# Optimization experiments

Measured on AMD Instinct MI355X. Metric: run time of the kernel, lower is better.

Reference implementation:

```python
import jax, jax.numpy as jnp
import numpy as np

N, E, IN, H, OUT, G = 100000, 1600000, 9, 64, 6, 1024
EPS = 1e-5


def setup_inputs() -> dict:
    key = jax.random.key(0)
    ks = jax.random.split(key, 24)
    inp = {
        "x": jax.random.normal(ks[0], (N, IN), dtype=jnp.float32),
        "edge_index": jax.random.randint(ks[1], (2, E), 0, N, dtype=jnp.int64),
        "edge_weight": jax.random.uniform(ks[2], (E,), dtype=jnp.float32),
        "batch": jnp.sort(jax.random.randint(ks[3], (N,), 0, G, dtype=jnp.int64)),
    }
    def lin(k, fan_in, fan_out):
        return jax.random.normal(k, (fan_in, fan_out), dtype=jnp.float32) / np.sqrt(fan_in)
    # GraphConv layer 0: IN -> H; layers 1,2: H -> H
    inp["W_rel0"], inp["W_root0"], inp["b0"] = lin(ks[4], IN, H), lin(ks[5], IN, H), jnp.zeros((H,), jnp.float32)
    inp["W_rel1"], inp["W_root1"], inp["b1"] = lin(ks[6], H, H), lin(ks[7], H, H), jnp.zeros((H,), jnp.float32)
    inp["W_rel2"], inp["W_root2"], inp["b2"] = lin(ks[8], H, H), lin(ks[9], H, H), jnp.zeros((H,), jnp.float32)
    # BatchNorm params for the first num_layers-1 = 2 layers
    inp["g0"], inp["be0"] = jnp.ones((H,), jnp.float32), jnp.zeros((H,), jnp.float32)
    inp["g1"], inp["be1"] = jnp.ones((H,), jnp.float32), jnp.zeros((H,), jnp.float32)
    # MLP head
    inp["W_l1"], inp["b_l1"] = lin(ks[10], H, H), jnp.zeros((H,), jnp.float32)
    inp["W_l2"], inp["b_l2"] = lin(ks[11], H, OUT), jnp.zeros((OUT,), jnp.float32)
    return inp


def graph_conv(x, src, dst, ew, W_rel, W_root, b):
    # PyG GraphConv: out = aggr_add(e_ji * x_j) @ W_rel + b + x @ W_root
    msg = x[src] * ew[:, None]                      # [E, F] gather
    agg = jax.ops.segment_sum(msg, dst, num_segments=x.shape[0])  # [N, F] scatter-add
    return agg @ W_rel + b + x @ W_root


def batch_norm(x, g, b):
    m = jnp.mean(x, axis=0)
    v = jnp.var(x, axis=0)
    return (x - m) * jax.lax.rsqrt(v + EPS) * g + b


def reference(x, edge_index, edge_weight, batch,
              W_rel0, W_root0, b0, W_rel1, W_root1, b1, W_rel2, W_root2, b2,
              g0, be0, g1, be1, W_l1, b_l1, W_l2, b_l2):
    src, dst = edge_index[0], edge_index[1]
    # layer 0: conv -> BN -> relu (dropout p applied only in training; eval here)
    h = graph_conv(x, src, dst, edge_weight, W_rel0, W_root0, b0)
    h = jax.nn.relu(batch_norm(h, g0, be0))
    # layer 1
    h = graph_conv(h, src, dst, edge_weight, W_rel1, W_root1, b1)
    h = jax.nn.relu(batch_norm(h, g1, be1))
    # layer 2 (no norm/relu)
    h = graph_conv(h, src, dst, edge_weight, W_rel2, W_root2, b2)
    # global mean pool over graphs
    summed = jax.ops.segment_sum(h, batch, num_segments=G)            # [G, H]
    counts = jax.ops.segment_sum(jnp.ones((h.shape[0],), h.dtype), batch, num_segments=G)
    pooled = summed / jnp.maximum(counts, 1.0)[:, None]
    # MLP head
    z = jax.nn.relu(pooled @ W_l1 + b_l1)
    return z @ W_l2 + b_l2
```

## Files before the change

### kernel.cpp

```cpp
#include <hip/hip_runtime.h>
#include <hip/hip_fp16.h>

constexpr int N    = 100000;
constexpr int E    = 1600000;
constexpr int FIN  = 9;
constexpr int OUTF = 6;
constexpr int G    = 1024;
constexpr int NPB  = 256;
constexpr int NB   = (N + NPB - 1) / NPB;
constexpr int CH   = 2048;
constexpr int NCH  = (E + CH - 1) / CH;
constexpr int BCAP = 4864;
constexpr int CBCAP= BCAP + NPB + 8;
constexpr int EBUF = 5888;
constexpr int ZCNT = 256 + G * 64;

typedef _Float16 f16x8 __attribute__((ext_vector_type(8)));
typedef float    f32x4 __attribute__((ext_vector_type(4)));

__device__ __forceinline__ void atomAddF(float* p, float v) { unsafeAtomicAdd(p, v); }

__device__ __forceinline__ float us2f(unsigned short u) {
    return __half2float(__builtin_bit_cast(__half, u));
}

__global__ __launch_bounds__(256) void initK(int* __restrict__ cursor, float* __restrict__ zeros,
    const float* __restrict__ x, __half* __restrict__ x9)
{
    int i = blockIdx.x * 256 + threadIdx.x;
    if (i < NB) cursor[i] = i * BCAP;
    if (i < ZCNT) zeros[i] = 0.f;
    if (i < N * FIN) x9[i] = __float2half(x[i]);
}

__global__ __launch_bounds__(256) void passA(const int* __restrict__ src, const int* __restrict__ dst,
    const float* __restrict__ ew, int* __restrict__ cursor, int2* __restrict__ bucketed)
{
    __shared__ int h[NB];
    __shared__ int hb[NB];
    int t = threadIdx.x;
    for (int i = t; i < NB; i += 256) h[i] = 0;
    __syncthreads();
    int base = blockIdx.x * CH;
    int myS[8], myD[8], rk[8]; float myW[8];
#pragma unroll
    for (int i = 0; i < 8; i++) {
        int e = base + i * 256 + t;
        if (e < E) {
            myS[i] = src[e]; myD[i] = dst[e]; myW[i] = ew[e];
            rk[i] = atomicAdd(&h[myD[i] >> 8], 1);
        } else myD[i] = -1;
    }
    __syncthreads();
    for (int i = t; i < NB; i += 256) hb[i] = h[i] ? atomicAdd(&cursor[i], h[i]) : 0;
    __syncthreads();
#pragma unroll
    for (int i = 0; i < 8; i++) if (myD[i] >= 0) {
        int packed = myS[i] | ((myD[i] & 255) << 24);
        bucketed[hb[myD[i] >> 8] + rk[i]] = make_int2(packed, __float_as_int(myW[i]));
    }
}

__global__ __launch_bounds__(NPB) void passB(const int* __restrict__ cursor,
    const int2* __restrict__ bucketed, int* __restrict__ ebeg, int* __restrict__ eend,
    int2* __restrict__ csr)
{
    __shared__ int2 ebuf[EBUF];
    __shared__ int cl[NPB], sa[NPB], sb[NPB], curs[NPB];
    int b = blockIdx.x, t = threadIdx.x;
    int node0 = b * NPB;
    int nnode = min(NPB, N - node0);
    int cnt = cursor[b] - b * BCAP;
    int abase = b * BCAP;
    int base = b * CBCAP;
    bool fits = (cnt <= EBUF);
    cl[t] = 0;
    __syncthreads();
    for (int e = t; e < cnt; e += NPB) {
        int2 r = bucketed[abase + e];
        if (fits) ebuf[e] = r;
        atomicAdd(&cl[((unsigned)r.x) >> 24], 1);
    }
    __syncthreads();
    int deg = cl[t];
    int pc = (deg + 1) & ~1;
    int* cur = sa; int* nxt = sb;
    cur[t] = pc;
    __syncthreads();
    for (int o = 1; o < NPB; o <<= 1) {
        int v = cur[t];
        if (t >= o) v += cur[t - o];
        nxt[t] = v;
        __syncthreads();
        int* tmp = cur; cur = nxt; nxt = tmp;
    }
    int off = cur[t] - pc;
    if (t < nnode) { ebeg[node0 + t] = base + off; eend[node0 + t] = base + off + deg; }
    curs[t] = off;
    __syncthreads();
    for (int e = t; e < cnt; e += NPB) {
        int2 r = fits ? ebuf[e] : bucketed[abase + e];
        int dl = ((unsigned)r.x) >> 24;
        int pos = base + atomicAdd(&curs[dl], 1);
        csr[pos] = make_int2(r.x & 0x00FFFFFF, r.y);
    }
    __syncthreads();
    if (t < nnode && (deg & 1)) csr[base + off + deg] = make_int2(0, 0);
    if (t < 4) csr[base + cur[NPB - 1] + t] = make_int2(0, 0);
}

__global__ __launch_bounds__(256) void wprep(const float* __restrict__ Wrel1, const float* __restrict__ Wroot1,
    const float* __restrict__ Wrel2, const float* __restrict__ Wroot2, __half* __restrict__ Wt)
{
    int i = blockIdx.x * 256 + threadIdx.x;
    int layer = i >> 13, r = i & 8191;
    int c = r >> 6, k = r & 63;
    const float* Wrel = layer ? Wrel2 : Wrel1;
    const float* Wroot = layer ? Wroot2 : Wroot1;
    float v = (c < 64) ? Wrel[k * 64 + c] : Wroot[k * 64 + (c - 64)];
    Wt[i] = __float2half(v);
}

__global__ __launch_bounds__(256, 2) void gather9(const __half* __restrict__ x9h,
    const int2* __restrict__ csr, const int* __restrict__ ebeg, const int* __restrict__ eend,
    float* __restrict__ agg9)
{
    const unsigned short* __restrict__ x9 = (const unsigned short*)x9h;
    int t = threadIdx.x, lane = t & 63;
    int es = lane >> 4, fc = min(lane & 15, FIN - 1);
    int wv = __builtin_amdgcn_readfirstlane((blockIdx.x * blockDim.x + t) >> 6);
    int nw = (gridDim.x * blockDim.x) >> 6;
    for (int n = wv; n < N; n += nw) {
        int beg = ebeg[n], end = eend[n];
        int last = end - 1;
        int2 eA0 = csr[min(beg + es,      last)];
        int2 eB0 = csr[min(beg + 4 + es,  last)];
        int2 eA1 = csr[min(beg + 8 + es,  last)];
        int2 eB1 = csr[min(beg + 12 + es, last)];
        unsigned short xA = x9[(size_t)eA0.x * FIN + fc];
        unsigned short xB = x9[(size_t)eB0.x * FIN + fc];
        float a0 = 0.f, a1 = 0.f;
        for (int k = beg; k < end; k += 8) {
            int2 eA2 = csr[min(k + 16 + es, last)];
            int2 eB2 = csr[min(k + 20 + es, last)];
            unsigned short nxA = x9[(size_t)eA1.x * FIN + fc];
            unsigned short nxB = x9[(size_t)eB1.x * FIN + fc];
            float wA = (k + es     < end) ? __int_as_float(eA0.y) : 0.f;
            float wB = (k + 4 + es < end) ? __int_as_float(eB0.y) : 0.f;
            a0 = fmaf(wA, us2f(xA), a0);
            a1 = fmaf(wB, us2f(xB), a1);
            eA0 = eA1; eB0 = eB1; eA1 = eA2; eB1 = eB2;
            xA = nxA; xB = nxB;
        }
        float r = a0 + a1;
        r += __shfl(r, lane ^ 16, 64);
        r += __shfl(r, lane ^ 32, 64);
        if (lane < FIN) agg9[(size_t)n * FIN + lane] = r;
    }
}

__global__ __launch_bounds__(256) void proj0post(const float* __restrict__ x,
    const float* __restrict__ agg9, const float* __restrict__ Wrel,
    const float* __restrict__ Wroot, const float* __restrict__ bias,
    __half* __restrict__ H0, float* __restrict__ stats)
{
    int t = threadIdx.x, j = t & 63;
    int nl = __builtin_amdgcn_readfirstlane(t >> 6);
    float wrel[FIN], wroot[FIN];
#pragma unroll
    for (int k = 0; k < FIN; k++) { wrel[k] = Wrel[k * 64 + j]; wroot[k] = Wroot[k * 64 + j]; }
    float bj = bias[j];
    float s1 = 0.f, s2 = 0.f;
    const int ntiles = N / 4;
    for (int tile = blockIdx.x; tile < ntiles; tile += gridDim.x) {
        int n = tile * 4 + nl;
        const float* xr = x + (size_t)n * FIN;
        const float* ar = agg9 + (size_t)n * FIN;
        float acc = bj;
#pragma unroll
        for (int k = 0; k < FIN; k++) {
            acc = fmaf(ar[k], wrel[k], acc);
            acc = fmaf(xr[k], wroot[k], acc);
        }
        H0[(size_t)n * 64 + j] = __float2half(acc);
        s1 += acc; s2 += acc * acc;
    }
    __shared__ float sred[256];
    sred[t] = s1; __syncthreads();
    if (t < 64) atomAddF(&stats[t], sred[t] + sred[t+64] + sred[t+128] + sred[t+192]);
    __syncthreads();
    sred[t] = s2; __syncthreads();
    if (t < 64) atomAddF(&stats[64 + t], sred[t] + sred[t+64] + sred[t+128] + sred[t+192]);
}

__global__ __launch_bounds__(256) void projm(const __half* __restrict__ Hin, const __half* __restrict__ Wt,
    const float* __restrict__ bias, const float* __restrict__ stats,
    const float* __restrict__ gam, const float* __restrict__ bet,
    __half* __restrict__ P, __half* __restrict__ Hout)
{
    int t = threadIdx.x, lane = t & 63;
    int wv = blockIdx.x * 4 + (t >> 6);
    int nw = gridDim.x * 4;
    int n16 = lane & 15, quad = lane >> 4;
    constexpr float invN = 1.0f / (float)N;
    float sc[16], sh[16];
#pragma unroll
    for (int jj = 0; jj < 16; jj++) {
        int k = (jj < 8) ? (quad * 8 + jj) : (32 + quad * 8 + (jj - 8));
        float m = stats[k] * invN;
        float v = stats[64 + k] * invN - m * m;
        sc[jj] = gam[k] * rsqrtf(v + 1e-5f);
        sh[jj] = bet[k] - m * sc[jj];
    }
    f16x8 bf[8][2];
#pragma unroll
    for (int ct = 0; ct < 8; ct++)
#pragma unroll
        for (int kh = 0; kh < 2; kh++)
            bf[ct][kh] = *(const f16x8*)(Wt + (size_t)(ct * 16 + n16) * 64 + kh * 32 + quad * 8);
    float bcol[4];
#pragma unroll
    for (int i = 0; i < 4; i++) bcol[i] = bias[i * 16 + n16];
    const int NT = N / 16;
    for (int tile = wv; tile < NT; tile += nw) {
        int n0 = tile * 16;
        f16x8 r0 = *(const f16x8*)(Hin + (size_t)(n0 + n16) * 64 + quad * 8);
        f16x8 r1 = *(const f16x8*)(Hin + (size_t)(n0 + n16) * 64 + 32 + quad * 8);
        f16x8 a0, a1;
#pragma unroll
        for (int jj = 0; jj < 8; jj++) {
            a0[jj] = (_Float16)fmaxf(fmaf((float)r0[jj], sc[jj],     sh[jj]),     0.f);
            a1[jj] = (_Float16)fmaxf(fmaf((float)r1[jj], sc[jj + 8], sh[jj + 8]), 0.f);
        }
        f32x4 acc[8];
#pragma unroll
        for (int ct = 0; ct < 8; ct++) {
            f32x4 c = {0.f, 0.f, 0.f, 0.f};
            c = __builtin_amdgcn_mfma_f32_16x16x32_f16(a0, bf[ct][0], c, 0, 0, 0);
            c = __builtin_amdgcn_mfma_f32_16x16x32_f16(a1, bf[ct][1], c, 0, 0, 0);
            acc[ct] = c;
        }
#pragma unroll
        for (int ct = 0; ct < 8; ct++) {
#pragma unroll
            for (int r = 0; r < 4; r++) {
                int n = n0 + quad * 4 + r;
                if (ct < 4) P[(size_t)n * 64 + ct * 16 + n16] = __float2half(acc[ct][r]);
                else Hout[(size_t)n * 64 + (ct - 4) * 16 + n16] = __float2half(acc[ct][r] + bcol[ct - 4]);
            }
        }
    }
}

template<int EPI>
__global__ __launch_bounds__(256, 2) void gather(const __half* __restrict__ Ph, __half* H,
    const int2* __restrict__ csr, const int* __restrict__ ebeg, const int* __restrict__ eend,
    float* __restrict__ stats, const int* __restrict__ batch, float* __restrict__ pool)
{
    const unsigned short* __restrict__ P = (const unsigned short*)Ph;
    int t = threadIdx.x, lane = t & 63;
    int wv = __builtin_amdgcn_readfirstlane((blockIdx.x * blockDim.x + t) >> 6);
    int nw = (gridDim.x * blockDim.x) >> 6;
    float s1 = 0.f, s2 = 0.f;
    const int NPAIR = N / 2;
    for (int pr = wv; pr < NPAIR; pr += nw) {
        int n0 = 2 * pr, n1 = n0 + 1;
        int b0 = ebeg[n0], m0 = (eend[n0] - b0 + 1) >> 1;
        int b1 = ebeg[n1], m1 = (eend[n1] - b1 + 1) >> 1;
        const int4* q0 = (const int4*)csr + (b0 >> 1);
        const int4* q1 = (const int4*)csr + (b1 >> 1);
        int c0 = max(m0 - 1, 0), c1 = max(m1 - 1, 0);
        float x0 = __half2float(H[(size_t)n0 * 64 + lane]);
        float x1 = __half2float(H[(size_t)n1 * 64 + lane]);
        int4 qaA = q0[0],          qbA = q0[min(1, c0)];
        int4 qcA = q1[0],          qdA = q1[min(1, c1)];
        int4 qaB = q0[min(2, c0)], qbB = q0[min(3, c0)];
        int4 qcB = q1[min(2, c1)], qdB = q1[min(3, c1)];
        int4 qaC = q0[min(4, c0)], qbC = q0[min(5, c0)];
        int4 qcC = q1[min(4, c1)], qdC = q1[min(5, c1)];
        unsigned short pa0 = P[(size_t)qaA.x * 64 + lane], pa1 = P[(size_t)qaA.z * 64 + lane];
        unsigned short pb0 = P[(size_t)qbA.x * 64 + lane], pb1 = P[(size_t)qbA.z * 64 + lane];
        unsigned short pc0 = P[(size_t)qcA.x * 64 + lane], pc1 = P[(size_t)qcA.z * 64 + lane];
        unsigned short pd0 = P[(size_t)qdA.x * 64 + lane], pd1 = P[(size_t)qdA.z * 64 + lane];
        unsigned short na0 = P[(size_t)qaB.x * 64 + lane], na1 = P[(size_t)qaB.z * 64 + lane];
        unsigned short nb0 = P[(size_t)qbB.x * 64 + lane], nb1 = P[(size_t)qbB.z * 64 + lane];
        unsigned short nc0 = P[(size_t)qcB.x * 64 + lane], nc1 = P[(size_t)qcB.z * 64 + lane];
        unsigned short nd0 = P[(size_t)qdB.x * 64 + lane], nd1 = P[(size_t)qdB.z * 64 + lane];
        float a0 = 0.f, a1 = 0.f, a2 = 0.f, a3 = 0.f;
        float a4 = 0.f, a5 = 0.f, a6 = 0.f, a7 = 0.f;
        int mm = max(m0, m1);
        for (int k = 0; k < mm; k += 2) {
            int4 qaD = q0[min(k + 6, c0)], qbD = q0[min(k + 7, c0)];
            int4 qcD = q1[min(k + 6, c1)], qdD = q1[min(k + 7, c1)];
            unsigned short ma0 = P[(size_t)qaC.x * 64 + lane], ma1 = P[(size_t)qaC.z * 64 + lane];
            unsigned short mb0 = P[(size_t)qbC.x * 64 + lane], mb1 = P[(size_t)qbC.z * 64 + lane];
            unsigned short mc0 = P[(size_t)qcC.x * 64 + lane], mc1 = P[(size_t)qcC.z * 64 + lane];
            unsigned short md0 = P[(size_t)qdC.x * 64 + lane], md1 = P[(size_t)qdC.z * 64 + lane];
            float wa = (k     < m0) ? __int_as_float(qaA.y) : 0.f;
            float wA = (k     < m0) ? __int_as_float(qaA.w) : 0.f;
            float wb = (k + 1 < m0) ? __int_as_float(qbA.y) : 0.f;
            float wB = (k + 1 < m0) ? __int_as_float(qbA.w) : 0.f;
            float wc = (k     < m1) ? __int_as_float(qcA.y) : 0.f;
            float wC = (k     < m1) ? __int_as_float(qcA.w) : 0.f;
            float wd = (k + 1 < m1) ? __int_as_float(qdA.y) : 0.f;
            float wD = (k + 1 < m1) ? __int_as_float(qdA.w) : 0.f;
            a0 = fmaf(wa, us2f(pa0), a0); a1 = fmaf(wA, us2f(pa1), a1);
            a2 = fmaf(wb, us2f(pb0), a2); a3 = fmaf(wB, us2f(pb1), a3);
            a4 = fmaf(wc, us2f(pc0), a4); a5 = fmaf(wC, us2f(pc1), a5);
            a6 = fmaf(wd, us2f(pd0), a6); a7 = fmaf(wD, us2f(pd1), a7);
            qaA = qaB; qbA = qbB; qcA = qcB; qdA = qdB;
            qaB = qaC; qbB = qbC; qcB = qcC; qdB = qdC;
            qaC = qaD; qbC = qbD; qcC = qcD; qdC = qdD;
            pa0 = na0; pa1 = na1; pb0 = nb0; pb1 = nb1;
            pc0 = nc0; pc1 = nc1; pd0 = nd0; pd1 = nd1;
            na0 = ma0; na1 = ma1; nb0 = mb0; nb1 = mb1;
            nc0 = mc0; nc1 = mc1; nd0 = md0; nd1 = md1;
        }
        float r0 = x0 + ((a0 + a2) + (a1 + a3));
        float r1 = x1 + ((a4 + a6) + (a5 + a7));
        if constexpr (EPI == 0) {
            H[(size_t)n0 * 64 + lane] = __float2half(r0);
            H[(size_t)n1 * 64 + lane] = __float2half(r1);
            s1 += r0 + r1; s2 += r0 * r0 + r1 * r1;
        } else {
            atomAddF(&pool[batch[n0] * 64 + lane], r0);
            atomAddF(&pool[batch[n1] * 64 + lane], r1);
        }
    }
    if constexpr (EPI == 0) {
        __shared__ float sred[256];
        sred[t] = s1; __syncthreads();
        if (t < 64) atomAddF(&stats[t], sred[t] + sred[t+64] + sred[t+128] + sred[t+192]);
        __syncthreads();
        sred[t] = s2; __syncthreads();
        if (t < 64) atomAddF(&stats[64 + t], sred[t] + sred[t+64] + sred[t+128] + sred[t+192]);
    }
}

__global__ __launch_bounds__(64) void head(const float* __restrict__ pool,
    const int* __restrict__ batch, const float* __restrict__ Wl1, const float* __restrict__ bl1,
    const float* __restrict__ Wl2, const float* __restrict__ bl2, float* __restrict__ out)
{
    int g = blockIdx.x, t = threadIdx.x;
    __shared__ float sp[64];
    __shared__ float sz[64];
    __shared__ int scnt;
    if (t == 0) {
        int lo = 0, hi = N;
        while (lo < hi) { int m = (lo + hi) >> 1; if (batch[m] < g) lo = m + 1; else hi = m; }
        int lo2 = lo, hi2 = N;
        while (lo2 < hi2) { int m = (lo2 + hi2) >> 1; if (batch[m] < g + 1) lo2 = m + 1; else hi2 = m; }
        scnt = lo2 - lo;
    }
    __syncthreads();
    float cnt = fmaxf((float)scnt, 1.0f);
    sp[t] = pool[g * 64 + t] / cnt;
    __syncthreads();
    float acc = bl1[t];
#pragma unroll
    for (int k = 0; k < 64; k++) acc = fmaf(sp[k], Wl1[k * 64 + t], acc);
    sz[t] = fmaxf(acc, 0.f);
    __syncthreads();
    if (t < OUTF) {
        float o = bl2[t];
#pragma unroll
        for (int k = 0; k < 64; k++) o = fmaf(sz[k], Wl2[k * OUTF + t], o);
        out[g * OUTF + t] = o;
    }
}

extern "C" void kernel_launch(void* const* d_in, const int* in_sizes, int n_in,
                              void* d_out, int out_size, void* d_ws, size_t ws_size,
                              hipStream_t stream)
{
    const float* x     = (const float*)d_in[0];
    const int*   ei    = (const int*)d_in[1];
    const float* ew    = (const float*)d_in[2];
    const int*   batch = (const int*)d_in[3];
    const float* Wrel0 = (const float*)d_in[4];
    const float* Wroot0= (const float*)d_in[5];
    const float* b0    = (const float*)d_in[6];
    const float* Wrel1 = (const float*)d_in[7];
    const float* Wroot1= (const float*)d_in[8];
    const float* b1    = (const float*)d_in[9];
    const float* Wrel2 = (const float*)d_in[10];
    const float* Wroot2= (const float*)d_in[11];
    const float* b2    = (const float*)d_in[12];
    const float* g0    = (const float*)d_in[13];
    const float* be0   = (const float*)d_in[14];
    const float* g1    = (const float*)d_in[15];
    const float* be1   = (const float*)d_in[16];
    const float* Wl1   = (const float*)d_in[17];
    const float* bl1   = (const float*)d_in[18];
    const float* Wl2   = (const float*)d_in[19];
    const float* bl2   = (const float*)d_in[20];
    const int* srcI = ei;
    const int* dstI = ei + E;

    __half* Ha     = (__half*)d_ws;
    __half* Hb     = Ha + (size_t)N * 64;
    __half* P      = Hb + (size_t)N * 64;
    int2*   csr    = (int2*)(P + (size_t)N * 64);
    int*    ebeg   = (int*)(csr + (size_t)NB * CBCAP);
    int*    eend   = ebeg + N;
    int*    cursor = eend + N;
    float*  stats0 = (float*)(cursor + NB);
    float*  stats1 = stats0 + 128;
    float*  pool   = stats1 + 128;
    __half* Wt1    = (__half*)(pool + G * 64);
    __half* Wt2    = Wt1 + 128 * 64;
    float*  agg9   = (float*)(Wt2 + 128 * 64);
    __half* x9     = (__half*)(agg9 + (size_t)N * FIN);
    int2*   bucketed = (int2*)Ha;

    initK<<<(N * FIN + 255) / 256, 256, 0, stream>>>(cursor, stats0, x, x9);
    passA<<<NCH, 256, 0, stream>>>(srcI, dstI, ew, cursor, bucketed);
    passB<<<NB, NPB, 0, stream>>>(cursor, bucketed, ebeg, eend, csr);
    wprep<<<64, 256, 0, stream>>>(Wrel1, Wroot1, Wrel2, Wroot2, Wt1);

    gather9<<<2048, 256, 0, stream>>>(x9, csr, ebeg, eend, agg9);
    proj0post<<<2048, 256, 0, stream>>>(x, agg9, Wrel0, Wroot0, b0, Ha, stats0);

    projm<<<1024, 256, 0, stream>>>(Ha, Wt1, b1, stats0, g0, be0, P, Hb);
    gather<0><<<2048, 256, 0, stream>>>(P, Hb, csr, ebeg, eend, stats1, nullptr, nullptr);

    projm<<<1024, 256, 0, stream>>>(Hb, Wt2, b2, stats1, g1, be1, P, Ha);
    gather<1><<<2048, 256, 0, stream>>>(P, Ha, csr, ebeg, eend, nullptr, batch, pool);

    head<<<G, 64, 0, stream>>>(pool, batch, Wl1, bl1, Wl2, bl2, (float*)d_out);
}
```

Baseline: 468.7 us.

## Stream gathered neighbor rows into LDS ring via global_load_lds pipeline

Rewrites the gather kernel so each wavefront runs a software-pipelined producer/consumer ring in shared memory. It issues direct global-to-LDS loads of neighbor feature rows (4 edges per step, GLK steps ahead) and consumes them after an explicit vmcnt wait. The old code held register-resident prefetch of two nodes at a time. The new scheme handles one node per iteration with a continuous cross-node prefetch stream, aiming to keep more memory requests in flight while cutting register pressure. The fixed vmcnt(8) count depends on exactly which loads are outstanding, so it is fragile. The extra LDS traffic and the dropped occupancy hint may also cost throughput.

```diff
diff --git a/kernel.cpp b/kernel.cpp
--- a/kernel.cpp
+++ b/kernel.cpp
@@ -22,6 +22,11 @@
 
 __device__ __forceinline__ float us2f(unsigned short u) {
     return __half2float(__builtin_bit_cast(__half, u));
+}
+
+__device__ __forceinline__ void gll4(const void* g, void* l) {
+    __builtin_amdgcn_global_load_lds((const __attribute__((address_space(1))) void*)g,
+                                     (__attribute__((address_space(3))) void*)l, 4, 0, 0);
 }
 
 __global__ __launch_bounds__(256) void initK(int* __restrict__ cursor, float* __restrict__ zeros,
@@ -252,83 +257,99 @@
     }
 }
 
+constexpr int GLK = 4;
+constexpr int GRS = 8;
+
 template<int EPI>
-__global__ __launch_bounds__(256, 2) void gather(const __half* __restrict__ Ph, __half* H,
+__global__ __launch_bounds__(256) void gather(const __half* __restrict__ Ph, __half* H,
     const int2* __restrict__ csr, const int* __restrict__ ebeg, const int* __restrict__ eend,
     float* __restrict__ stats, const int* __restrict__ batch, float* __restrict__ pool)
 {
-    const unsigned short* __restrict__ P = (const unsigned short*)Ph;
-    int t = threadIdx.x, lane = t & 63;
+    __shared__ unsigned short ring[4][GRS][256];
+    __shared__ int4 pring[4][GRS][2];
+    __shared__ float sred[256];
+    int t = threadIdx.x, lane = t & 63, w = t >> 6;
+    unsigned short* myring = &ring[w][0][0];
+    int4* mypring = &pring[w][0][0];
+    const char* Pb = (const char*)Ph;
+    const int4* csr4 = (const int4*)csr;
     int wv = __builtin_amdgcn_readfirstlane((blockIdx.x * blockDim.x + t) >> 6);
     int nw = (gridDim.x * blockDim.x) >> 6;
+    int l31 = (lane & 31) * 4;
+
+    int pn = pn = wv, ppb = 0, ppm = 0, pnq = 0, pq = 0;
+    {
+        int b = ebeg[pn]; ppb = b >> 1; ppm = (eend[pn] - b + 1) >> 1; pnq = (ppm + 1) >> 1;
+        while (pnq == 0) {
+            pn += nw; if (pn >= N) break;
+            int b2 = ebeg[pn]; ppb = b2 >> 1; ppm = (eend[pn] - b2 + 1) >> 1; pnq = (ppm + 1) >> 1;
+        }
+    }
+    auto produceStep = [&](int slot) {
+        if (pn < N) {
+            int lastpk = ppb + ppm - 1;
+            int4 pk0 = csr4[min(ppb + 2 * pq,     lastpk)];
+            int4 pk1 = csr4[min(ppb + 2 * pq + 1, lastpk)];
+            int r0 = (lane < 32) ? pk0.x : pk0.z;
+            int r1 = (lane < 32) ? pk1.x : pk1.z;
+            gll4(Pb + (size_t)r0 * 128 + l31, myring + slot * 256);
+            gll4(Pb + (size_t)r1 * 128 + l31, myring + slot * 256 + 128);
+            if (lane < 2) mypring[slot * 2 + lane] = lane ? pk1 : pk0;
+            pq++;
+            if (pq >= pnq) {
+                pq = 0;
+                do {
+                    pn += nw; if (pn >= N) break;
+                    int b = ebeg[pn]; ppb = b >> 1; ppm = (eend[pn] - b + 1) >> 1; pnq = (ppm + 1) >> 1;
+                } while (pnq == 0);
+            }
+        } else {
+            gll4(Pb + l31, myring + slot * 256);
+            gll4(Pb + l31, myring + slot * 256 + 128);
+        }
+    };
+
+    int qp = 0, qc = 0;
+    for (int i = 0; i < GLK; i++) { produceStep(qp & (GRS - 1)); qp++; }
+
     float s1 = 0.f, s2 = 0.f;
-    const int NPAIR = N / 2;
-    for (int pr = wv; pr < NPAIR; pr += nw) {
-        int n0 = 2 * pr, n1 = n0 + 1;
-        int b0 = ebeg[n0], m0 = (eend[n0] - b0 + 1) >> 1;
-        int b1 = ebeg[n1], m1 = (eend[n1] - b1 + 1) >> 1;
-        const int4* q0 = (const int4*)csr + (b0 >> 1);
-        const int4* q1 = (const int4*)csr + (b1 >> 1);
-        int c0 = max(m0 - 1, 0), c1 = max(m1 - 1, 0);
-        float x0 = __half2float(H[(size_t)n0 * 64 + lane]);
-        float x1 = __half2float(H[(size_t)n1 * 64 + lane]);
-        int4 qaA = q0[0],          qbA = q0[min(1, c0)];
-        int4 qcA = q1[0],          qdA = q1[min(1, c1)];
-        int4 qaB = q0[min(2, c0)], qbB = q0[min(3, c0)];
-        int4 qcB = q1[min(2, c1)], qdB = q1[min(3, c1)];
-        int4 qaC = q0[min(4, c0)], qbC = q0[min(5, c0)];
-        int4 qcC = q1[min(4, c1)], qdC = q1[min(5, c1)];
-        unsigned short pa0 = P[(size_t)qaA.x * 64 + lane], pa1 = P[(size_t)qaA.z * 64 + lane];
-        unsigned short pb0 = P[(size_t)qbA.x * 64 + lane], pb1 = P[(size_t)qbA.z * 64 + lane];
-        unsigned short pc0 = P[(size_t)qcA.x * 64 + lane], pc1 = P[(size_t)qcA.z * 64 + lane];
-        unsigned short pd0 = P[(size_t)qdA.x * 64 + lane], pd1 = P[(size_t)qdA.z * 64 + lane];
-        unsigned short na0 = P[(size_t)qaB.x * 64 + lane], na1 = P[(size_t)qaB.z * 64 + lane];
-        unsigned short nb0 = P[(size_t)qbB.x * 64 + lane], nb1 = P[(size_t)qbB.z * 64 + lane];
-        unsigned short nc0 = P[(size_t)qcB.x * 64 + lane], nc1 = P[(size_t)qcB.z * 64 + lane];
-        unsigned short nd0 = P[(size_t)qdB.x * 64 + lane], nd1 = P[(size_t)qdB.z * 64 + lane];
-        float a0 = 0.f, a1 = 0.f, a2 = 0.f, a3 = 0.f;
-        float a4 = 0.f, a5 = 0.f, a6 = 0.f, a7 = 0.f;
-        int mm = max(m0, m1);
-        for (int k = 0; k < mm; k += 2) {
-            int4 qaD = q0[min(k + 6, c0)], qbD = q0[min(k + 7, c0)];
-            int4 qcD = q1[min(k + 6, c1)], qdD = q1[min(k + 7, c1)];
-            unsigned short ma0 = P[(size_t)qaC.x * 64 + lane], ma1 = P[(size_t)qaC.z * 64 + lane];
-            unsigned short mb0 = P[(size_t)qbC.x * 64 + lane], mb1 = P[(size_t)qbC.z * 64 + lane];
-            unsigned short mc0 = P[(size_t)qcC.x * 64 + lane], mc1 = P[(size_t)qcC.z * 64 + lane];
-            unsigned short md0 = P[(size_t)qdC.x * 64 + lane], md1 = P[(size_t)qdC.z * 64 + lane];
-            float wa = (k     < m0) ? __int_as_float(qaA.y) : 0.f;
-            float wA = (k     < m0) ? __int_as_float(qaA.w) : 0.f;
-            float wb = (k + 1 < m0) ? __int_as_float(qbA.y) : 0.f;
-            float wB = (k + 1 < m0) ? __int_as_float(qbA.w) : 0.f;
-            float wc = (k     < m1) ? __int_as_float(qcA.y) : 0.f;
-            float wC = (k     < m1) ? __int_as_float(qcA.w) : 0.f;
-            float wd = (k + 1 < m1) ? __int_as_float(qdA.y) : 0.f;
-            float wD = (k + 1 < m1) ? __int_as_float(qdA.w) : 0.f;
-            a0 = fmaf(wa, us2f(pa0), a0); a1 = fmaf(wA, us2f(pa1), a1);
-            a2 = fmaf(wb, us2f(pb0), a2); a3 = fmaf(wB, us2f(pb1), a3);
-            a4 = fmaf(wc, us2f(pc0), a4); a5 = fmaf(wC, us2f(pc1), a5);
-            a6 = fmaf(wd, us2f(pd0), a6); a7 = fmaf(wD, us2f(pd1), a7);
-            qaA = qaB; qbA = qbB; qcA = qcB; qdA = qdB;
-            qaB = qaC; qbB = qbC; qcB = qcC; qdB = qdC;
-            qaC = qaD; qbC = qbD; qcC = qcD; qdC = qdD;
-            pa0 = na0; pa1 = na1; pb0 = nb0; pb1 = nb1;
-            pc0 = nc0; pc1 = nc1; pd0 = nd0; pd1 = nd1;
-            na0 = ma0; na1 = ma1; nb0 = mb0; nb1 = mb1;
-            nc0 = mc0; nc1 = mc1; nd0 = md0; nd1 = md1;
-        }
-        float r0 = x0 + ((a0 + a2) + (a1 + a3));
-        float r1 = x1 + ((a4 + a6) + (a5 + a7));
+    for (int cn = wv; cn < N; cn += nw) {
+        int b = ebeg[cn];
+        int cm = (eend[cn] - b + 1) >> 1;
+        int cnq = (cm + 1) >> 1;
+        float xr = __half2float(H[(size_t)cn * 64 + lane]);
+        float acc = 0.f;
+        for (int q = 0; q < cnq; q++) {
+            produceStep(qp & (GRS - 1)); qp++;
+            int slot = qc & (GRS - 1); qc++;
+            asm volatile("s_waitcnt vmcnt(8)" ::: "memory");
+            int4 pk0 = mypring[slot * 2];
+            int4 pk1 = mypring[slot * 2 + 1];
+            const unsigned short* s = myring + slot * 256;
+            float v0 = us2f(s[lane]);
+            float v1 = us2f(s[64 + lane]);
+            float v2 = us2f(s[128 + lane]);
+            float v3 = us2f(s[192 + lane]);
+            float w0 = (2 * q     < cm) ? __int_as_float(pk0.y) : 0.f;
+            float w1 = (2 * q     < cm) ? __int_as_float(pk0.w) : 0.f;
+            float w2 = (2 * q + 1 < cm) ? __int_as_float(pk1.y) : 0.f;
+            float w3 = (2 * q + 1 < cm) ? __int_as_float(pk1.w) : 0.f;
+            acc = fmaf(w0, v0, acc);
+            acc = fmaf(w1, v1, acc);
+            acc = fmaf(w2, v2, acc);
+            acc = fmaf(w3, v3, acc);
+        }
+        float r = xr + acc;
         if constexpr (EPI == 0) {
-            H[(size_t)n0 * 64 + lane] = __float2half(r0);
-            H[(size_t)n1 * 64 + lane] = __float2half(r1);
-            s1 += r0 + r1; s2 += r0 * r0 + r1 * r1;
+            H[(size_t)cn * 64 + lane] = __float2half(r);
+            s1 += r; s2 += r * r;
         } else {
-            atomAddF(&pool[batch[n0] * 64 + lane], r0);
-            atomAddF(&pool[batch[n1] * 64 + lane], r1);
-        }
-    }
+            atomAddF(&pool[batch[cn] * 64 + lane], r);
+        }
+    }
+    asm volatile("s_waitcnt vmcnt(0)" ::: "memory");
+
     if constexpr (EPI == 0) {
-        __shared__ float sred[256];
         sred[t] = s1; __syncthreads();
         if (t < 64) atomAddF(&stats[t], sred[t] + sred[t+64] + sred[t+128] + sred[t+192]);
         __syncthreads();
```

Result: slower. 687.3 us (+46.6%).

## Partition each node's edges into source slices and gather slice-by-slice for locality

Applied to the files above, without the earlier changes.

The CSR build now sorts each node's edges into four source-index slices, each padded to even length, and records the slice boundaries per node. The 64-wide gather kernels make each wave own 13 nodes and walk them slice by slice, so all waves touch the same quarter of P at the same time. This should improve L2/MALL hit rates for the random row gathers. It also pads x9 to 16 halves per row so gather9 uses aligned row addresses, at the cost of extra padding edges, a more complex passB, and lower memory-level parallelism per wave in the gather loop.

```diff
diff --git a/kernel.cpp b/kernel.cpp
--- a/kernel.cpp
+++ b/kernel.cpp
@@ -11,7 +11,9 @@
 constexpr int CH   = 2048;
 constexpr int NCH  = (E + CH - 1) / CH;
 constexpr int BCAP = 4864;
-constexpr int CBCAP= BCAP + NPB + 8;
+constexpr int NSLC = 4;
+constexpr int SLCW = (N + NSLC - 1) / NSLC;
+constexpr int CBCAP= BCAP + NPB * NSLC + 8;
 constexpr int EBUF = 5888;
 constexpr int ZCNT = 256 + G * 64;
 
@@ -30,7 +32,10 @@
     int i = blockIdx.x * 256 + threadIdx.x;
     if (i < NB) cursor[i] = i * BCAP;
     if (i < ZCNT) zeros[i] = 0.f;
-    if (i < N * FIN) x9[i] = __float2half(x[i]);
+    if (i < N * 16) {
+        int n = i >> 4, f = i & 15;
+        x9[i] = __float2half(f < FIN ? x[n * FIN + f] : 0.f);
+    }
 }
 
 __global__ __launch_bounds__(256) void passA(const int* __restrict__ src, const int* __restrict__ dst,
@@ -63,10 +68,11 @@
 
 __global__ __launch_bounds__(NPB) void passB(const int* __restrict__ cursor,
     const int2* __restrict__ bucketed, int* __restrict__ ebeg, int* __restrict__ eend,
-    int2* __restrict__ csr)
+    int4* __restrict__ segpk, int2* __restrict__ csr)
 {
     __shared__ int2 ebuf[EBUF];
-    __shared__ int cl[NPB], sa[NPB], sb[NPB], curs[NPB];
+    __shared__ int cl4[NPB][NSLC];
+    __shared__ int sa[NPB], sb[NPB];
     int b = blockIdx.x, t = threadIdx.x;
     int node0 = b * NPB;
     int nnode = min(NPB, N - node0);
@@ -74,16 +80,19 @@
     int abase = b * BCAP;
     int base = b * CBCAP;
     bool fits = (cnt <= EBUF);
-    cl[t] = 0;
+#pragma unroll
+    for (int s = 0; s < NSLC; s++) cl4[t][s] = 0;
     __syncthreads();
     for (int e = t; e < cnt; e += NPB) {
         int2 r = bucketed[abase + e];
         if (fits) ebuf[e] = r;
-        atomicAdd(&cl[((unsigned)r.x) >> 24], 1);
-    }
-    __syncthreads();
-    int deg = cl[t];
-    int pc = (deg + 1) & ~1;
+        int src = r.x & 0x00FFFFFF;
+        atomicAdd(&cl4[((unsigned)r.x) >> 24][src / SLCW], 1);
+    }
+    __syncthreads();
+    int d0 = cl4[t][0], d1 = cl4[t][1], d2 = cl4[t][2], d3 = cl4[t][3];
+    int p0 = (d0 + 1) & ~1, p1 = (d1 + 1) & ~1, p2 = (d2 + 1) & ~1, p3 = (d3 + 1) & ~1;
+    int pc = p0 + p1 + p2 + p3;
     int* cur = sa; int* nxt = sb;
     cur[t] = pc;
     __syncthreads();
@@ -95,17 +104,31 @@
         int* tmp = cur; cur = nxt; nxt = tmp;
     }
     int off = cur[t] - pc;
-    if (t < nnode) { ebeg[node0 + t] = base + off; eend[node0 + t] = base + off + deg; }
-    curs[t] = off;
+    if (t < nnode) {
+        ebeg[node0 + t] = base + off;
+        eend[node0 + t] = base + off + pc;
+        segpk[node0 + t] = make_int4(p0 >> 1, (p0 + p1) >> 1,
+                                     (p0 + p1 + p2) >> 1, pc >> 1);
+    }
+    cl4[t][0] = off;
+    cl4[t][1] = off + p0;
+    cl4[t][2] = off + p0 + p1;
+    cl4[t][3] = off + p0 + p1 + p2;
     __syncthreads();
     for (int e = t; e < cnt; e += NPB) {
         int2 r = fits ? ebuf[e] : bucketed[abase + e];
         int dl = ((unsigned)r.x) >> 24;
-        int pos = base + atomicAdd(&curs[dl], 1);
-        csr[pos] = make_int2(r.x & 0x00FFFFFF, r.y);
-    }
-    __syncthreads();
-    if (t < nnode && (deg & 1)) csr[base + off + deg] = make_int2(0, 0);
+        int src = r.x & 0x00FFFFFF;
+        int pos = base + atomicAdd(&cl4[dl][src / SLCW], 1);
+        csr[pos] = make_int2(src, r.y);
+    }
+    __syncthreads();
+    if (t < nnode) {
+        if (d0 & 1) csr[base + cl4[t][0]] = make_int2(0, 0);
+        if (d1 & 1) csr[base + cl4[t][1]] = make_int2(0, 0);
+        if (d2 & 1) csr[base + cl4[t][2]] = make_int2(0, 0);
+        if (d3 & 1) csr[base + cl4[t][3]] = make_int2(0, 0);
+    }
     if (t < 4) csr[base + cur[NPB - 1] + t] = make_int2(0, 0);
 }
 
@@ -127,7 +150,7 @@
 {
     const unsigned short* __restrict__ x9 = (const unsigned short*)x9h;
     int t = threadIdx.x, lane = t & 63;
-    int es = lane >> 4, fc = min(lane & 15, FIN - 1);
+    int es = lane >> 4, fc = lane & 15;
     int wv = __builtin_amdgcn_readfirstlane((blockIdx.x * blockDim.x + t) >> 6);
     int nw = (gridDim.x * blockDim.x) >> 6;
     for (int n = wv; n < N; n += nw) {
@@ -137,14 +160,14 @@
         int2 eB0 = csr[min(beg + 4 + es,  last)];
         int2 eA1 = csr[min(beg + 8 + es,  last)];
         int2 eB1 = csr[min(beg + 12 + es, last)];
-        unsigned short xA = x9[(size_t)eA0.x * FIN + fc];
-        unsigned short xB = x9[(size_t)eB0.x * FIN + fc];
+        unsigned short xA = x9[(size_t)eA0.x * 16 + fc];
+        unsigned short xB = x9[(size_t)eB0.x * 16 + fc];
         float a0 = 0.f, a1 = 0.f;
         for (int k = beg; k < end; k += 8) {
             int2 eA2 = csr[min(k + 16 + es, last)];
             int2 eB2 = csr[min(k + 20 + es, last)];
-            unsigned short nxA = x9[(size_t)eA1.x * FIN + fc];
-            unsigned short nxB = x9[(size_t)eB1.x * FIN + fc];
+            unsigned short nxA = x9[(size_t)eA1.x * 16 + fc];
+            unsigned short nxB = x9[(size_t)eB1.x * 16 + fc];
             float wA = (k + es     < end) ? __int_as_float(eA0.y) : 0.f;
             float wB = (k + 4 + es < end) ? __int_as_float(eB0.y) : 0.f;
             a0 = fmaf(wA, us2f(xA), a0);
@@ -254,85 +277,60 @@
 
 template<int EPI>
 __global__ __launch_bounds__(256, 2) void gather(const __half* __restrict__ Ph, __half* H,
-    const int2* __restrict__ csr, const int* __restrict__ ebeg, const int* __restrict__ eend,
+    const int2* __restrict__ csr, const int* __restrict__ ebeg, const int4* __restrict__ segpk,
     float* __restrict__ stats, const int* __restrict__ batch, float* __restrict__ pool)
 {
     const unsigned short* __restrict__ P = (const unsigned short*)Ph;
     int t = threadIdx.x, lane = t & 63;
     int wv = __builtin_amdgcn_readfirstlane((blockIdx.x * blockDim.x + t) >> 6);
     int nw = (gridDim.x * blockDim.x) >> 6;
-    float s1 = 0.f, s2 = 0.f;
-    const int NPAIR = N / 2;
-    for (int pr = wv; pr < NPAIR; pr += nw) {
-        int n0 = 2 * pr, n1 = n0 + 1;
-        int b0 = ebeg[n0], m0 = (eend[n0] - b0 + 1) >> 1;
-        int b1 = ebeg[n1], m1 = (eend[n1] - b1 + 1) >> 1;
-        const int4* q0 = (const int4*)csr + (b0 >> 1);
-        const int4* q1 = (const int4*)csr + (b1 >> 1);
-        int c0 = max(m0 - 1, 0), c1 = max(m1 - 1, 0);
-        float x0 = __half2float(H[(size_t)n0 * 64 + lane]);
-        float x1 = __half2float(H[(size_t)n1 * 64 + lane]);
-        int4 qaA = q0[0],          qbA = q0[min(1, c0)];
-        int4 qcA = q1[0],          qdA = q1[min(1, c1)];
-        int4 qaB = q0[min(2, c0)], qbB = q0[min(3, c0)];
-        int4 qcB = q1[min(2, c1)], qdB = q1[min(3, c1)];
-        int4 qaC = q0[min(4, c0)], qbC = q0[min(5, c0)];
-        int4 qcC = q1[min(4, c1)], qdC = q1[min(5, c1)];
-        unsigned short pa0 = P[(size_t)qaA.x * 64 + lane], pa1 = P[(size_t)qaA.z * 64 + lane];
-        unsigned short pb0 = P[(size_t)qbA.x * 64 + lane], pb1 = P[(size_t)qbA.z * 64 + lane];
-        unsigned short pc0 = P[(size_t)qcA.x * 64 + lane], pc1 = P[(size_t)qcA.z * 64 + lane];
-        unsigned short pd0 = P[(size_t)qdA.x * 64 + lane], pd1 = P[(size_t)qdA.z * 64 + lane];
-        unsigned short na0 = P[(size_t)qaB.x * 64 + lane], na1 = P[(size_t)qaB.z * 64 + lane];
-        unsigned short nb0 = P[(size_t)qbB.x * 64 + lane], nb1 = P[(size_t)qbB.z * 64 + lane];
-        unsigned short nc0 = P[(size_t)qcB.x * 64 + lane], nc1 = P[(size_t)qcB.z * 64 + lane];
-        unsigned short nd0 = P[(size_t)qdB.x * 64 + lane], nd1 = P[(size_t)qdB.z * 64 + lane];
-        float a0 = 0.f, a1 = 0.f, a2 = 0.f, a3 = 0.f;
-        float a4 = 0.f, a5 = 0.f, a6 = 0.f, a7 = 0.f;
-        int mm = max(m0, m1);
-        for (int k = 0; k < mm; k += 2) {
-            int4 qaD = q0[min(k + 6, c0)], qbD = q0[min(k + 7, c0)];
-            int4 qcD = q1[min(k + 6, c1)], qdD = q1[min(k + 7, c1)];
-            unsigned short ma0 = P[(size_t)qaC.x * 64 + lane], ma1 = P[(size_t)qaC.z * 64 + lane];
-            unsigned short mb0 = P[(size_t)qbC.x * 64 + lane], mb1 = P[(size_t)qbC.z * 64 + lane];
-            unsigned short mc0 = P[(size_t)qcC.x * 64 + lane], mc1 = P[(size_t)qcC.z * 64 + lane];
-            unsigned short md0 = P[(size_t)qdC.x * 64 + lane], md1 = P[(size_t)qdC.z * 64 + lane];
-            float wa = (k     < m0) ? __int_as_float(qaA.y) : 0.f;
-            float wA = (k     < m0) ? __int_as_float(qaA.w) : 0.f;
-            float wb = (k + 1 < m0) ? __int_as_float(qbA.y) : 0.f;
-            float wB = (k + 1 < m0) ? __int_as_float(qbA.w) : 0.f;
-            float wc = (k     < m1) ? __int_as_float(qcA.y) : 0.f;
-            float wC = (k     < m1) ? __int_as_float(qcA.w) : 0.f;
-            float wd = (k + 1 < m1) ? __int_as_float(qdA.y) : 0.f;
-            float wD = (k + 1 < m1) ? __int_as_float(qdA.w) : 0.f;
-            a0 = fmaf(wa, us2f(pa0), a0); a1 = fmaf(wA, us2f(pa1), a1);
-            a2 = fmaf(wb, us2f(pb0), a2); a3 = fmaf(wB, us2f(pb1), a3);
-            a4 = fmaf(wc, us2f(pc0), a4); a5 = fmaf(wC, us2f(pc1), a5);
-            a6 = fmaf(wd, us2f(pd0), a6); a7 = fmaf(wD, us2f(pd1), a7);
-            qaA = qaB; qbA = qbB; qcA = qcB; qdA = qdB;
-            qaB = qaC; qbB = qbC; qcB = qcC; qdB = qdC;
-            qaC = qaD; qbC = qbD; qcC = qcD; qdC = qdD;
-            pa0 = na0; pa1 = na1; pb0 = nb0; pb1 = nb1;
-            pc0 = nc0; pc1 = nc1; pd0 = nd0; pd1 = nd1;
-            na0 = ma0; na1 = ma1; nb0 = mb0; nb1 = mb1;
-            nc0 = mc0; nc1 = mc1; nd0 = md0; nd1 = md1;
-        }
-        float r0 = x0 + ((a0 + a2) + (a1 + a3));
-        float r1 = x1 + ((a4 + a6) + (a5 + a7));
-        if constexpr (EPI == 0) {
-            H[(size_t)n0 * 64 + lane] = __float2half(r0);
-            H[(size_t)n1 * 64 + lane] = __float2half(r1);
-            s1 += r0 + r1; s2 += r0 * r0 + r1 * r1;
-        } else {
-            atomAddF(&pool[batch[n0] * 64 + lane], r0);
-            atomAddF(&pool[batch[n1] * 64 + lane], r1);
+    constexpr int NN = 13;
+    float acc[NN];
+#pragma unroll
+    for (int i = 0; i < NN; i++) acc[i] = 0.f;
+    const int4* csr4 = (const int4*)csr;
+#pragma unroll
+    for (int p = 0; p < NSLC; p++) {
+#pragma unroll
+        for (int i = 0; i < NN; i++) {
+            int n = wv + i * nw;
+            if (n < N) {
+                int e4 = ebeg[n] >> 1;
+                int4 pf = segpk[n];
+                int s0 = (p == 0) ? 0 : (p == 1 ? pf.x : p == 2 ? pf.y : pf.z);
+                int s1 = (p == 0) ? pf.x : (p == 1 ? pf.y : p == 2 ? pf.z : pf.w);
+                const int4* q = csr4 + e4;
+                float a0 = 0.f, a1 = 0.f;
+#pragma unroll 2
+                for (int k = s0; k < s1; k++) {
+                    int4 pk = q[k];
+                    a0 = fmaf(__int_as_float(pk.y), us2f(P[(size_t)pk.x * 64 + lane]), a0);
+                    a1 = fmaf(__int_as_float(pk.w), us2f(P[(size_t)pk.z * 64 + lane]), a1);
+                }
+                acc[i] += a0 + a1;
+            }
+        }
+    }
+    float s1s = 0.f, s2s = 0.f;
+#pragma unroll
+    for (int i = 0; i < NN; i++) {
+        int n = wv + i * nw;
+        if (n < N) {
+            float r = __half2float(H[(size_t)n * 64 + lane]) + acc[i];
+            if constexpr (EPI == 0) {
+                H[(size_t)n * 64 + lane] = __float2half(r);
+                s1s += r; s2s += r * r;
+            } else {
+                atomAddF(&pool[batch[n] * 64 + lane], r);
+            }
         }
     }
     if constexpr (EPI == 0) {
         __shared__ float sred[256];
-        sred[t] = s1; __syncthreads();
+        sred[t] = s1s; __syncthreads();
         if (t < 64) atomAddF(&stats[t], sred[t] + sred[t+64] + sred[t+128] + sred[t+192]);
         __syncthreads();
-        sred[t] = s2; __syncthreads();
+        sred[t] = s2s; __syncthreads();
         if (t < 64) atomAddF(&stats[64 + t], sred[t] + sred[t+64] + sred[t+128] + sred[t+192]);
     }
 }
@@ -403,7 +401,8 @@
     int2*   csr    = (int2*)(P + (size_t)N * 64);
     int*    ebeg   = (int*)(csr + (size_t)NB * CBCAP);
     int*    eend   = ebeg + N;
-    int*    cursor = eend + N;
+    int4*   segpk  = (int4*)(eend + N);
+    int*    cursor = (int*)(segpk + N);
     float*  stats0 = (float*)(cursor + NB);
     float*  stats1 = stats0 + 128;
     float*  pool   = stats1 + 128;
@@ -413,19 +412,19 @@
     __half* x9     = (__half*)(agg9 + (size_t)N * FIN);
     int2*   bucketed = (int2*)Ha;
 
-    initK<<<(N * FIN + 255) / 256, 256, 0, stream>>>(cursor, stats0, x, x9);
+    initK<<<(N * 16 + 255) / 256, 256, 0, stream>>>(cursor, stats0, x, x9);
     passA<<<NCH, 256, 0, stream>>>(srcI, dstI, ew, cursor, bucketed);
-    passB<<<NB, NPB, 0, stream>>>(cursor, bucketed, ebeg, eend, csr);
+    passB<<<NB, NPB, 0, stream>>>(cursor, bucketed, ebeg, eend, segpk, csr);
     wprep<<<64, 256, 0, stream>>>(Wrel1, Wroot1, Wrel2, Wroot2, Wt1);
 
     gather9<<<2048, 256, 0, stream>>>(x9, csr, ebeg, eend, agg9);
     proj0post<<<2048, 256, 0, stream>>>(x, agg9, Wrel0, Wroot0, b0, Ha, stats0);
 
     projm<<<1024, 256, 0, stream>>>(Ha, Wt1, b1, stats0, g0, be0, P, Hb);
-    gather<0><<<2048, 256, 0, stream>>>(P, Hb, csr, ebeg, eend, stats1, nullptr, nullptr);
+    gather<0><<<2048, 256, 0, stream>>>(P, Hb, csr, ebeg, segpk, stats1, nullptr, nullptr);
 
     projm<<<1024, 256, 0, stream>>>(Hb, Wt2, b2, stats1, g1, be1, P, Ha);
-    gather<1><<<2048, 256, 0, stream>>>(P, Ha, csr, ebeg, eend, nullptr, batch, pool);
+    gather<1><<<2048, 256, 0, stream>>>(P, Ha, csr, ebeg, segpk, nullptr, batch, pool);
 
     head<<<G, 64, 0, stream>>>(pool, batch, Wl1, bl1, Wl2, bl2, (float*)d_out);
 }
```

Result: slower. 568.7 us (+21.3%).
